# Optimization experiments

Measured on AMD Instinct MI355X. Metric: run time of the kernel, lower is better.

The kernel has to match this reference:

```python
import jax, jax.numpy as jnp
import numpy as np

G = 16  # self.group
K = 3   # unfold/fold kernel size


def setup_inputs() -> dict:
    key = jax.random.key(0)
    feature = jax.random.normal(key, (2, 128, 192, 192), dtype=jnp.float32)
    return {"feature": feature}


def reference(feature):
    B, C, H, W = feature.shape
    Cg = C // G
    Hm, Wm = H - K + 1, W - K + 1
    L = Hm * Wm

    # --- nn.Unfold(kernel_size=3), all groups at once ---
    # patches[b, c, k, y, x] with k = ki*3 + kj (channel-major flat = c*9 + k)
    slices = [feature[:, :, ki:ki + Hm, kj:kj + Wm] for ki in range(K) for kj in range(K)]
    patches = jnp.stack(slices, axis=2)                 # [B, C, 9, Hm, Wm]
    # per-group series flat dim is Cg*9 (order cg*9+k); chunk(9) -> reshape [9, Cg]
    motif = patches.reshape(B, G, Cg * 9, L).reshape(B, G, 9, Cg, L)  # [B,G,9,Cg,L]

    # --- cdist + diag=inf + argmin (squared distances: same argmin as p=2) ---
    gram = jnp.einsum('bgjcl,bgjdl->bgjcd', motif, motif)   # [B,G,9,Cg,Cg]
    sq = jnp.einsum('bgjcl,bgjcl->bgjc', motif, motif)      # [B,G,9,Cg]
    d2 = sq[..., :, None] + sq[..., None, :] - 2.0 * gram
    eye = jnp.eye(Cg, dtype=bool)
    d2 = jnp.where(eye, jnp.inf, d2)
    nn_idx = jnp.argmin(d2, axis=-1)                        # [B,G,9,Cg] int

    # --- torch.unique loop overwrites motif_new: only the LAST (max) unique
    # index and its count survive ---
    u_max = jnp.max(nn_idx, axis=-1)                        # [B,G,9]
    c_max = jnp.sum(nn_idx == u_max[..., None], axis=-1).astype(feature.dtype)  # [B,G,9]

    motif_nn = jnp.take_along_axis(motif, u_max[..., None, None], axis=3)  # [B,G,9,1,L]
    # float '//' in torch is floor division
    term = jnp.floor(motif * motif_nn * c_max[..., None, None] / Cg)
    # l == 0 branch drops the '+ motif' term
    batch_mask = (jnp.arange(B) != 0).astype(feature.dtype).reshape(B, 1, 1, 1, 1)
    out_ser = motif * batch_mask + term                     # [B,G,9,Cg,L]

    # --- nn.Fold: input layout reinterpreted as (channel, kernel) flat = c*9+k ---
    ser2 = out_ser.reshape(B, G, 9 * Cg, L).reshape(B, G, Cg, 9, Hm, Wm)
    out = jnp.zeros((B, G, Cg, H, W), feature.dtype)
    for k in range(K * K):
        ki, kj = k // K, k % K
        out = out.at[:, :, :, ki:ki + Hm, kj:kj + Wm].add(ser2[:, :, :, k])
    return out.reshape(B, C, H, W)
```

## Files before the change

### kernel.cpp

```cpp
#include <hip/hip_runtime.h>
#include <hip/hip_bf16.h>
#include <math.h>

#define BB 2
#define CC 128
#define GG 16
#define CG 8
#define HH 192
#define WW 192
#define HM 190
#define WM 190
#define LL (HM * WM)
#define HWSZ (HH * WW)
#define NTRIPLE (BB * GG * 9)
#define SPLIT 6
#define SLICE_LEN ((LL + SPLIT - 1) / SPLIT)

__device__ float g_part[NTRIPLE * SPLIT * 36];
__device__ int g_rel[BB * GG * 72];
__device__ float g_scl[BB * GG * 72];

__global__ __launch_bounds__(256) void phase1a_kernel(
    const float* __restrict__ feat) {
  const int tri = blockIdx.x / SPLIT;
  const int sl = blockIdx.x % SPLIT;
  const int b = tri / (GG * 9);
  const int rem = tri % (GG * 9);
  const int g = rem / 9;
  const int j = rem % 9;

  const float* base[8];
#pragma unroll
  for (int d = 0; d < 8; ++d) {
    const int f = j * 8 + d;
    const int c = f / 9;
    const int k = f % 9;
    const int ki = k / 3, kj = k % 3;
    base[d] = feat + (size_t)(b * CC + g * CG + c) * HWSZ + ki * WW + kj;
  }

  float acc[36];
#pragma unroll
  for (int i = 0; i < 36; ++i) acc[i] = 0.0f;

  const int l0 = sl * SLICE_LEN;
  const int l1 = (l0 + SLICE_LEN < LL) ? (l0 + SLICE_LEN) : LL;
  for (int l = l0 + (int)threadIdx.x; l < l1; l += 256) {
    const int y = l / WM;
    const int x = l - y * WM;
    const int off = y * WW + x;
    float v[8];
#pragma unroll
    for (int d = 0; d < 8; ++d) v[d] = base[d][off];
#pragma unroll
    for (int d = 0; d < 8; ++d) acc[d] += v[d] * v[d];
    int p = 8;
#pragma unroll
    for (int c = 0; c < 8; ++c)
#pragma unroll
      for (int d = c + 1; d < 8; ++d) acc[p++] += v[c] * v[d];
  }

  __shared__ float red[36 * 4];
  const int lane = threadIdx.x & 63;
  const int wave = threadIdx.x >> 6;
#pragma unroll
  for (int i = 0; i < 36; ++i) {
    float v = acc[i];
    for (int o = 32; o > 0; o >>= 1) v += __shfl_down(v, o, 64);
    if (lane == 0) red[i * 4 + wave] = v;
  }
  __syncthreads();
  if (threadIdx.x < 36) {
    const int i = threadIdx.x;
    g_part[(tri * SPLIT + sl) * 36 + i] =
        red[i * 4] + red[i * 4 + 1] + red[i * 4 + 2] + red[i * 4 + 3];
  }
}

__global__ __launch_bounds__(64) void phase1b_kernel() {
  const int tri = blockIdx.x * 64 + (int)threadIdx.x;
  if (tri >= NTRIPLE) return;
  const int b = tri / (GG * 9);
  const int rem = tri % (GG * 9);
  const int g = rem / 9;
  const int j = rem % 9;

  float tot[36];
#pragma unroll
  for (int i = 0; i < 36; ++i) tot[i] = 0.0f;
  for (int s = 0; s < SPLIT; ++s)
#pragma unroll
    for (int i = 0; i < 36; ++i) tot[i] += g_part[(tri * SPLIT + s) * 36 + i];

  float sq[8], gm[8][8];
#pragma unroll
  for (int i = 0; i < 8; ++i) sq[i] = tot[i];
  {
    int p = 8;
    for (int c = 0; c < 8; ++c)
      for (int d = c + 1; d < 8; ++d) {
        gm[c][d] = tot[p];
        gm[d][c] = tot[p];
        ++p;
      }
  }
  int nn[8];
  for (int c = 0; c < 8; ++c) {
    float best = INFINITY;
    int bi = 0;
    for (int d = 0; d < 8; ++d) {
      if (d == c) continue;
      const float d2 = sq[c] + sq[d] - 2.0f * gm[c][d];
      if (d2 < best) {
        best = d2;
        bi = d;
      }
    }
    nn[c] = bi;
  }
  int um = 0;
  for (int c = 0; c < 8; ++c) um = um > nn[c] ? um : nn[c];
  int cnt = 0;
  for (int c = 0; c < 8; ++c) cnt += (nn[c] == um) ? 1 : 0;

  const float sc = (float)cnt * 0.125f;
  const int fn = j * 8 + um;
  const int cn = fn / 9;
  const int kn = fn % 9;
  const int kin = kn / 3, kjn = kn % 3;
  for (int d = 0; d < 8; ++d) {
    const int f = j * 8 + d;
    const int cl = f / 9;
    const int k = f % 9;
    const int ki = k / 3, kj = k % 3;
    const int rel = (cn - cl) * HWSZ + (kin - ki) * WW + (kjn - kj);
    const int tix = (b * GG + g) * 72 + f;
    g_rel[tix] = rel;
    g_scl[tix] = sc;
  }
}

__global__ __launch_bounds__(256) void phase2_kernel(
    const float* __restrict__ feat, float* __restrict__ out) {
  const int row = blockIdx.x * 4 + ((int)threadIdx.x >> 6);
  const int lane = (int)threadIdx.x & 63;
  const int plane = row / HH;
  const int h = row % HH;
  const int b = plane / CC;
  const int ch = plane % CC;
  const int g = ch >> 3;
  const int cl = ch & 7;

  const int tbase = (b * GG + g) * 72 + cl * 9;
  const float* rowp = feat + (size_t)plane * HWSZ + h * WW;
  float* orow = out + (size_t)plane * HWSZ + h * WW;
  const float* rowlane = rowp + lane;

  const float v0 = rowlane[0];
  const float v1 = rowlane[64];
  const float v2 = rowlane[128];
  float a0 = 0.0f, a1 = 0.0f, a2 = 0.0f;

#pragma unroll
  for (int k = 0; k < 9; ++k) {
    const int ki = k / 3, kj = k % 3;
    const bool hv = (h >= ki) & (h < HM + ki);
    if (hv) {
      const int oo = g_rel[tbase + k];
      const float sc = g_scl[tbase + k];
      const bool wv0 = (lane >= kj);
      const bool wv2 = (lane < 62 + kj);
      const int o0 = wv0 ? oo : 0;
      const int o2 = wv2 ? oo : 0;
      const float n0 = rowlane[o0];
      const float n1 = rowlane[oo + 64];
      const float n2 = rowlane[o2 + 128];
      const float t0 = floorf(v0 * n0 * sc);
      const float t1 = floorf(v1 * n1 * sc);
      const float t2 = floorf(v2 * n2 * sc);
      a0 += wv0 ? t0 : 0.0f;
      a1 += t1;
      a2 += wv2 ? t2 : 0.0f;
    }
  }

  if (b != 0) {
    const int chn = (h < 2 ? h : 2) - (h > 189 ? h - 189 : 0) + 1;
    const int w0 = lane, w2 = lane + 128;
    const int cw0 = (w0 < 2 ? w0 : 2) + 1;
    const int cw2 = 3 - (w2 > 189 ? w2 - 189 : 0);
    a0 += (float)(chn * cw0) * v0;
    a1 += (float)(chn * 3) * v1;
    a2 += (float)(chn * cw2) * v2;
  }
  orow[0 + lane] = a0;
  orow[64 + lane] = a1;
  orow[128 + lane] = a2;
}

extern "C" void kernel_launch(void* const* d_in, const int* in_sizes, int n_in,
                              void* d_out, int out_size, void* d_ws,
                              size_t ws_size, hipStream_t stream) {
  const float* feat = (const float*)d_in[0];
  float* out = (float*)d_out;
  (void)d_ws;
  (void)ws_size;

  phase1a_kernel<<<NTRIPLE * SPLIT, 256, 0, stream>>>(feat);
  phase1b_kernel<<<(NTRIPLE + 63) / 64, 64, 0, stream>>>();

  const int rows = BB * CC * HH;
  phase2_kernel<<<rows / 4, 256, 0, stream>>>(feat, out);
}
```

Measured before the change: 145.7 us.

## Vectorize phase1 reductions and split phase2 into float4 interior and edge kernels

Phase1a now partitions work by row blocks and loads float4 vectors per channel, handling the row tail by zeroing overlapping lanes. This removes the per-element divide and scalar loads. Phase2 is split into an interior kernel that processes four pixels per thread with vector loads and no bounds checks, plus a separate edge kernel for border pixels with full validity masking. This adds an extra launch, and the interior blocks have many early-exiting threads, in exchange for wider memory accesses and less branching.

```diff
diff --git a/kernel.cpp b/kernel.cpp
--- a/kernel.cpp
+++ b/kernel.cpp
@@ -14,7 +14,10 @@
 #define HWSZ (HH * WW)
 #define NTRIPLE (BB * GG * 9)
 #define SPLIT 6
-#define SLICE_LEN ((LL + SPLIT - 1) / SPLIT)
+#define ROWS_PER_SLICE 32
+
+typedef float float4a __attribute__((ext_vector_type(4), aligned(4)));
+typedef float float4v __attribute__((ext_vector_type(4)));
 
 __device__ float g_part[NTRIPLE * SPLIT * 36];
 __device__ int g_rel[BB * GG * 72];
@@ -43,22 +46,39 @@
 #pragma unroll
   for (int i = 0; i < 36; ++i) acc[i] = 0.0f;
 
-  const int l0 = sl * SLICE_LEN;
-  const int l1 = (l0 + SLICE_LEN < LL) ? (l0 + SLICE_LEN) : LL;
-  for (int l = l0 + (int)threadIdx.x; l < l1; l += 256) {
-    const int y = l / WM;
-    const int x = l - y * WM;
-    const int off = y * WW + x;
-    float v[8];
-#pragma unroll
-    for (int d = 0; d < 8; ++d) v[d] = base[d][off];
-#pragma unroll
-    for (int d = 0; d < 8; ++d) acc[d] += v[d] * v[d];
+  const int y0 = sl * ROWS_PER_SLICE;
+  const int y1 = (y0 + ROWS_PER_SLICE < HM) ? y0 + ROWS_PER_SLICE : HM;
+  const int ng = (y1 - y0) * 48;
+
+  for (int gi = (int)threadIdx.x; gi < ng; gi += 256) {
+    const int y = y0 + gi / 48;
+    const int xg = gi % 48;
+    const bool tail = (xg == 47);
+    const int xL = tail ? 186 : xg * 4;
+    const int ro = y * WW + xL;
+    float4a v[8];
+#pragma unroll
+    for (int d = 0; d < 8; ++d) v[d] = *(const float4a*)(base[d] + ro);
+    if (tail) {
+#pragma unroll
+      for (int d = 0; d < 8; ++d) {
+        v[d].x = 0.0f;
+        v[d].y = 0.0f;
+      }
+    }
+#pragma unroll
+    for (int d = 0; d < 8; ++d)
+      acc[d] += v[d].x * v[d].x + v[d].y * v[d].y + v[d].z * v[d].z +
+                v[d].w * v[d].w;
     int p = 8;
 #pragma unroll
     for (int c = 0; c < 8; ++c)
 #pragma unroll
-      for (int d = c + 1; d < 8; ++d) acc[p++] += v[c] * v[d];
+      for (int d = c + 1; d < 8; ++d) {
+        acc[p] += v[c].x * v[d].x + v[c].y * v[d].y + v[c].z * v[d].z +
+                  v[c].w * v[d].w;
+        ++p;
+      }
   }
 
   __shared__ float red[36 * 4];
@@ -141,62 +161,93 @@
   }
 }
 
-__global__ __launch_bounds__(256) void phase2_kernel(
+__global__ __launch_bounds__(256) void phase2_main_kernel(
     const float* __restrict__ feat, float* __restrict__ out) {
-  const int row = blockIdx.x * 4 + ((int)threadIdx.x >> 6);
-  const int lane = (int)threadIdx.x & 63;
-  const int plane = row / HH;
-  const int h = row % HH;
-  const int b = plane / CC;
-  const int ch = plane % CC;
-  const int g = ch >> 3;
-  const int cl = ch & 7;
-
-  const int tbase = (b * GG + g) * 72 + cl * 9;
-  const float* rowp = feat + (size_t)plane * HWSZ + h * WW;
-  float* orow = out + (size_t)plane * HWSZ + h * WW;
-  const float* rowlane = rowp + lane;
-
-  const float v0 = rowlane[0];
-  const float v1 = rowlane[64];
-  const float v2 = rowlane[128];
-  float a0 = 0.0f, a1 = 0.0f, a2 = 0.0f;
-
+  const int plane = blockIdx.x / 36;
+  const int inner = (blockIdx.x % 36) * 1024 + (int)threadIdx.x * 4;
+  const int h = inner / WW;
+  const int w0 = inner % WW;
+  if (h < 2 || h >= HM || w0 < 4 || w0 >= 188) return;
+
+  const int g = (plane % CC) >> 3;
+  const int cl = (plane % CC) & 7;
+  const int tbase = ((plane / CC) * GG + g) * 72 + cl * 9;
+
+  int rel[9];
+  float scl[9];
+#pragma unroll
+  for (int k = 0; k < 9; ++k) {
+    rel[k] = g_rel[tbase + k];
+    scl[k] = g_scl[tbase + k];
+  }
+
+  const float* p = feat + (size_t)plane * HWSZ + inner;
+  const float4v v = *(const float4v*)p;
+  float4v acc = {0.0f, 0.0f, 0.0f, 0.0f};
+#pragma unroll
+  for (int k = 0; k < 9; ++k) {
+    const float4a n = *(const float4a*)(p + rel[k]);
+    const float s = scl[k];
+    acc.x += floorf(v.x * n.x * s);
+    acc.y += floorf(v.y * n.y * s);
+    acc.z += floorf(v.z * n.z * s);
+    acc.w += floorf(v.w * n.w * s);
+  }
+  if (plane >= CC) {
+    acc.x += 9.0f * v.x;
+    acc.y += 9.0f * v.y;
+    acc.z += 9.0f * v.z;
+    acc.w += 9.0f * v.w;
+  }
+  *(float4v*)(out + (size_t)plane * HWSZ + inner) = acc;
+}
+
+__global__ __launch_bounds__(256) void phase2_edge_kernel(
+    const float* __restrict__ feat, float* __restrict__ out) {
+  const int gid = blockIdx.x * 256 + (int)threadIdx.x;
+  const int plane = gid / 2272;
+  const int ei = gid % 2272;
+  int h, w;
+  if (ei < 768) {
+    const int r = ei / WW;
+    h = (r < 2) ? r : r + 188;
+    w = ei % WW;
+  } else {
+    const int e2 = ei - 768;
+    h = 2 + (e2 >> 3);
+    const int w8 = e2 & 7;
+    w = (w8 < 4) ? w8 : w8 + 184;
+  }
+  const int g = (plane % CC) >> 3;
+  const int cl = (plane % CC) & 7;
+  const int tbase = ((plane / CC) * GG + g) * 72 + cl * 9;
+
+  int rel[9];
+  float scl[9];
+#pragma unroll
+  for (int k = 0; k < 9; ++k) {
+    rel[k] = g_rel[tbase + k];
+    scl[k] = g_scl[tbase + k];
+  }
+
+  const int idx = plane * HWSZ + h * WW + w;
+  const float* p = feat + idx;
+  const float v = *p;
+  float acc = 0.0f;
+  int nv = 0;
 #pragma unroll
   for (int k = 0; k < 9; ++k) {
     const int ki = k / 3, kj = k % 3;
-    const bool hv = (h >= ki) & (h < HM + ki);
-    if (hv) {
-      const int oo = g_rel[tbase + k];
-      const float sc = g_scl[tbase + k];
-      const bool wv0 = (lane >= kj);
-      const bool wv2 = (lane < 62 + kj);
-      const int o0 = wv0 ? oo : 0;
-      const int o2 = wv2 ? oo : 0;
-      const float n0 = rowlane[o0];
-      const float n1 = rowlane[oo + 64];
-      const float n2 = rowlane[o2 + 128];
-      const float t0 = floorf(v0 * n0 * sc);
-      const float t1 = floorf(v1 * n1 * sc);
-      const float t2 = floorf(v2 * n2 * sc);
-      a0 += wv0 ? t0 : 0.0f;
-      a1 += t1;
-      a2 += wv2 ? t2 : 0.0f;
-    }
-  }
-
-  if (b != 0) {
-    const int chn = (h < 2 ? h : 2) - (h > 189 ? h - 189 : 0) + 1;
-    const int w0 = lane, w2 = lane + 128;
-    const int cw0 = (w0 < 2 ? w0 : 2) + 1;
-    const int cw2 = 3 - (w2 > 189 ? w2 - 189 : 0);
-    a0 += (float)(chn * cw0) * v0;
-    a1 += (float)(chn * 3) * v1;
-    a2 += (float)(chn * cw2) * v2;
-  }
-  orow[0 + lane] = a0;
-  orow[64 + lane] = a1;
-  orow[128 + lane] = a2;
+    const int y = h - ki, x = w - kj;
+    const bool valid = ((unsigned)y < (unsigned)HM) & ((unsigned)x < (unsigned)WM);
+    const int o = valid ? rel[k] : 0;
+    const float n = p[o];
+    const float fl = floorf(v * n * scl[k]);
+    acc += valid ? fl : 0.0f;
+    nv += valid ? 1 : 0;
+  }
+  if (plane >= CC) acc += (float)nv * v;
+  out[idx] = acc;
 }
 
 extern "C" void kernel_launch(void* const* d_in, const int* in_sizes, int n_in,
@@ -210,6 +261,6 @@
   phase1a_kernel<<<NTRIPLE * SPLIT, 256, 0, stream>>>(feat);
   phase1b_kernel<<<(NTRIPLE + 63) / 64, 64, 0, stream>>>();
 
-  const int rows = BB * CC * HH;
-  phase2_kernel<<<rows / 4, 256, 0, stream>>>(feat, out);
-}
+  phase2_main_kernel<<<BB * CC * 36, 256, 0, stream>>>(feat, out);
+  phase2_edge_kernel<<<2272, 256, 0, stream>>>(feat, out);
+}
```

Result: faster. 140.6 us (-3.5%).
